# Optimization experiments

Measured on AMD Instinct MI355X. Metric: run time of the kernel, lower is better.

## Reference

```python
import jax, jax.numpy as jnp
import numpy as np

NEG_SLOPE = 0.2

def symlog(v):
    return jnp.sign(v) * jnp.log1p(jnp.abs(v))

def conv1d(v, w, b):
    # v: (N, Cin, L), w: (Cout, Cin, 3), 'same' padding, stride 1
    out = jax.lax.conv_general_dilated(v, w, (1,), 'SAME',
                                       dimension_numbers=('NCH', 'OIH', 'NCH'))
    return out + b[None, :, None]

def glorot(key, shape, fan_in, fan_out):
    s = jnp.sqrt(6.0 / (fan_in + fan_out))
    return jax.random.uniform(key, shape, jnp.float32, -s, s)

def setup_inputs() -> dict:
    N, L, E = 20000, 128, 320000
    IN, H, C, OHC = 512, 8, 32, 8
    key = jax.random.key(0)
    ks = jax.random.split(key, 12)
    x = jax.random.normal(ks[0], (N, IN), jnp.float32)
    onehot = jax.random.uniform(ks[1], (N, L), jnp.float32)
    src = jax.random.randint(ks[2], (E,), 0, N)
    off = jax.random.randint(ks[3], (E,), 1, N)
    dst = (src + off) % N  # guarantees no self loops
    adj = jnp.stack([src, dst], axis=0).astype(jnp.int64)
    lin_w = glorot(ks[4], (IN + OHC, H * C), IN + OHC, H * C)
    att_l = glorot(ks[5], (1, H, C), C, C)
    att_r = glorot(ks[6], (1, H, C), C, C)
    bias = jnp.zeros((H * C,), jnp.float32)
    conv1_w = glorot(ks[7], (8, 1, 3), 3, 24)
    conv1_b = jnp.zeros((8,), jnp.float32)
    conv2_w = glorot(ks[8], (16, 8, 3), 24, 48)
    conv2_b = jnp.zeros((16,), jnp.float32)
    lin2_w = glorot(ks[9], (16, OHC), 16, OHC)
    lin2_b = jnp.zeros((OHC,), jnp.float32)
    return {"x": x, "onehot": onehot, "adj": adj, "n_nodes": N,
            "lin_w": lin_w, "att_l": att_l, "att_r": att_r, "bias": bias,
            "conv1_w": conv1_w, "conv1_b": conv1_b,
            "conv2_w": conv2_w, "conv2_b": conv2_b,
            "lin2_w": lin2_w, "lin2_b": lin2_b}

def reference(x, onehot, adj, n_nodes, lin_w, att_l, att_r, bias,
              conv1_w, conv1_b, conv2_w, conv2_b, lin2_w, lin2_b):
    N = n_nodes
    H, C = att_l.shape[1], att_l.shape[2]
    # one-hot conv pipe: sort -> symlog -> conv-relu x2 -> global avg pool -> linear
    prepared = symlog(jnp.sort(onehot, axis=-1))[:, None, :]  # (N,1,L)
    h = jax.nn.relu(conv1d(prepared, conv1_w, conv1_b))
    h = jax.nn.relu(conv1d(h, conv2_w, conv2_b))
    readout = h.mean(axis=-1) @ lin2_w + lin2_b  # (N, OHC)
    xin = jnp.concatenate([x, readout], axis=-1)
    xh = (xin @ lin_w).reshape(N, H, C)
    al = (xh * att_l).sum(axis=-1)  # (N,H) sending alphas
    ar = (xh * att_r).sum(axis=-1)  # (N,H) receiving alphas
    # add self loops (input adj has none, so remove_self_loops is a no-op)
    loops = jnp.arange(N, dtype=adj.dtype)
    src = jnp.concatenate([adj[0], loops])
    dst = jnp.concatenate([adj[1], loops])
    # GAT-style attention with segment softmax over receiving nodes
    alpha = jax.nn.leaky_relu(al[src] + ar[dst], NEG_SLOPE)  # (Etot,H)
    amax = jax.ops.segment_max(alpha, dst, num_segments=N)
    ex = jnp.exp(alpha - amax[dst])
    denom = jax.ops.segment_sum(ex, dst, num_segments=N)
    alpha = ex / denom[dst]
    # weight + scatter-add aggregate
    wx = xh[src] * alpha[..., None]  # (Etot,H,C)
    new_x = jax.ops.segment_sum(wx, dst, num_segments=N).reshape(N, H * C) + bias
    new_onehot = jax.ops.segment_sum(onehot[src], dst, num_segments=N) + onehot
    return new_x, new_onehot
```

## Files before the change

### kernel.cpp

```cpp
#include <hip/hip_runtime.h>

#define NEG_SLOPE 0.2f

typedef __attribute__((ext_vector_type(4))) float f32x4;
typedef __attribute__((ext_vector_type(2))) float f32x2;
typedef __attribute__((ext_vector_type(8))) short short8;

__device__ __forceinline__ f32x2 mk2(float a, float b) { f32x2 r; r[0] = a; r[1] = b; return r; }

__device__ __forceinline__ f32x2 FMA2(f32x2 a, f32x2 b, f32x2 c) {
#if __has_builtin(__builtin_elementwise_fma)
    return __builtin_elementwise_fma(a, b, c);
#else
    f32x2 r; r[0] = fmaf(a[0], b[0], c[0]); r[1] = fmaf(a[1], b[1], c[1]); return r;
#endif
}

__device__ __forceinline__ ushort f2bf(float f) {
    uint u = __float_as_uint(f);
    u += 0x7FFFu + ((u >> 16) & 1u);
    return (ushort)(u >> 16);
}
__device__ __forceinline__ float bflo(uint u) { return __uint_as_float(u << 16); }
__device__ __forceinline__ float bfhi(uint u) { return __uint_as_float(u & 0xffff0000u); }

__global__ __launch_bounds__(256) void k_conv_wave(
    const float* __restrict__ x, const float* __restrict__ onehot,
    const float* __restrict__ c1w, const float* __restrict__ c1b,
    const float* __restrict__ c2w, const float* __restrict__ c2b,
    const float* __restrict__ l2w, const float* __restrict__ l2b,
    ushort* __restrict__ xpad, uint* __restrict__ ohb, int* __restrict__ cursor, int N) {
    __shared__ ushort Hall[4][1056];

    const int gid = blockIdx.x * 256 + threadIdx.x;
    if (gid < N) cursor[gid] = 0;

    const int wave = threadIdx.x >> 6;
    const int lane = threadIdx.x & 63;
    const int n = blockIdx.x * 4 + wave;
    if (n >= N) return;
    ushort* H = Hall[wave];

    {
        const float* xp = &x[(size_t)n*512 + lane*8];
        float4 lo = *reinterpret_cast<const float4*>(xp);
        float4 hi = *reinterpret_cast<const float4*>(xp + 4);
        uint4 w;
        w.x = (uint)f2bf(lo.x) | ((uint)f2bf(lo.y) << 16);
        w.y = (uint)f2bf(lo.z) | ((uint)f2bf(lo.w) << 16);
        w.z = (uint)f2bf(hi.x) | ((uint)f2bf(hi.y) << 16);
        w.w = (uint)f2bf(hi.z) | ((uint)f2bf(hi.w) << 16);
        *reinterpret_cast<uint4*>(&xpad[(size_t)n*544 + lane*8]) = w;
        if (lane < 3) {
            const uint4 z = make_uint4(0,0,0,0);
            *reinterpret_cast<uint4*>(&xpad[(size_t)n*544 + 520 + lane*8]) = z;
        }
    }

    float2 in2 = *reinterpret_cast<const float2*>(&onehot[(size_t)n * 128 + lane * 2]);
    ohb[(size_t)n*64 + lane] = (uint)f2bf(in2.x) | ((uint)f2bf(in2.y) << 16);
    float v0 = log1pf(in2.x);
    float v1 = log1pf(in2.y);

    #pragma unroll
    for (int k = 2; k <= 128; k <<= 1) {
        const bool asc = ((lane & (k >> 1)) == 0);
        #pragma unroll
        for (int j = k >> 1; j >= 2; j >>= 1) {
            const int m = j >> 1;
            float p0 = __shfl_xor(v0, m, 64);
            float p1 = __shfl_xor(v1, m, 64);
            const bool keepmin = (((lane & m) == 0) == asc);
            v0 = keepmin ? fminf(v0, p0) : fmaxf(v0, p0);
            v1 = keepmin ? fminf(v1, p1) : fmaxf(v1, p1);
        }
        float lo = fminf(v0, v1), hi = fmaxf(v0, v1);
        v0 = asc ? lo : hi;
        v1 = asc ? hi : lo;
    }

    float pm = __shfl_up(v1, 1, 64); if (lane == 0)  pm = 0.f;
    float pp = __shfl_down(v0, 1, 64); if (lane == 63) pp = 0.f;

    float h0[8], h1[8];
    {
        const f32x2 xm = mk2(pm, v0), x0 = mk2(v0, v1), xp2 = mk2(v1, pp);
        #pragma unroll
        for (int c = 0; c < 8; ++c) {
            const float w0 = c1w[c*3+0], w1 = c1w[c*3+1], w2 = c1w[c*3+2], b = c1b[c];
            f32x2 h = FMA2(xm, mk2(w0, w0), FMA2(x0, mk2(w1, w1), FMA2(xp2, mk2(w2, w2), mk2(b, b))));
            h0[c] = fmaxf(h[0], 0.f);
            h1[c] = fmaxf(h[1], 0.f);
        }
    }

    {
        if (lane == 0) {
            const uint4 z = make_uint4(0,0,0,0);
            *reinterpret_cast<uint4*>(&H[0*8])   = z;
            *reinterpret_cast<uint4*>(&H[130*8]) = z;
            *reinterpret_cast<uint4*>(&H[65*8])  = z;
        }
        uint4 w0, w1;
        w0.x = (uint)f2bf(h0[0]) | ((uint)f2bf(h0[1]) << 16);
        w0.y = (uint)f2bf(h0[2]) | ((uint)f2bf(h0[3]) << 16);
        w0.z = (uint)f2bf(h0[4]) | ((uint)f2bf(h0[5]) << 16);
        w0.w = (uint)f2bf(h0[6]) | ((uint)f2bf(h0[7]) << 16);
        w1.x = (uint)f2bf(h1[0]) | ((uint)f2bf(h1[1]) << 16);
        w1.y = (uint)f2bf(h1[2]) | ((uint)f2bf(h1[3]) << 16);
        w1.z = (uint)f2bf(h1[4]) | ((uint)f2bf(h1[5]) << 16);
        w1.w = (uint)f2bf(h1[6]) | ((uint)f2bf(h1[7]) << 16);
        *reinterpret_cast<uint4*>(&H[(66 + lane)*8]) = w0;
        *reinterpret_cast<uint4*>(&H[(lane + 1)*8])  = w1;
    }

    const int co = lane & 15;
    const int g2 = lane >> 4;
    short8 bfrag;
    #pragma unroll
    for (int j = 0; j < 8; ++j) bfrag[j] = 0;
    if (g2 < 3) {
        #pragma unroll
        for (int j = 0; j < 8; ++j) bfrag[j] = (short)f2bf(c2w[(co*8 + j)*3 + g2]);
    }
    const float bias_c = c2b[co];
    const f32x4 zacc = (f32x4)0.f;

    float poolv = 0.f;
    #pragma unroll
    for (int s = 0; s < 8; ++s) {
        const int q = s*16 + co + g2;
        const int slot = (q >> 1) + (q & 1)*66;
        short8 afrag = *reinterpret_cast<const short8*>(&H[slot*8]);
        f32x4 d = __builtin_amdgcn_mfma_f32_16x16x32_bf16(afrag, bfrag, zacc, 0, 0, 0);
        poolv += fmaxf(d[0] + bias_c, 0.f);
        poolv += fmaxf(d[1] + bias_c, 0.f);
        poolv += fmaxf(d[2] + bias_c, 0.f);
        poolv += fmaxf(d[3] + bias_c, 0.f);
    }
    poolv += __shfl_xor(poolv, 16, 64);
    poolv += __shfl_xor(poolv, 32, 64);

    float r = (lane < 8) ? l2b[lane] : 0.f;
    #pragma unroll
    for (int c = 0; c < 16; ++c) {
        float pc = __shfl(poolv, c, 64);
        if (lane < 8) r = fmaf(pc * (1.f/128.f), l2w[c*8 + lane], r);
    }
    if (lane < 8) xpad[(size_t)n*544 + 512 + lane] = f2bf(r);
}

__global__ __launch_bounds__(256) void k_prep(
    const float* __restrict__ lin_w, ushort* __restrict__ Bt,
    const int* __restrict__ dst, int* __restrict__ cursor, int E) {
    const int gid = blockIdx.x * 256 + threadIdx.x;
    if (gid < E) atomicAdd(&cursor[dst[gid]], 1);
    const int col = blockIdx.x;
    if (col < 256) {
        for (int k = threadIdx.x; k < 544; k += 256) {
            float v = (k < 520) ? lin_w[(size_t)k*256 + col] : 0.f;
            Bt[(size_t)col*544 + k] = f2bf(v);
        }
    }
}

__global__ __launch_bounds__(1024) void k_scan(int* __restrict__ deg, int* __restrict__ row_start, int N) {
    __shared__ int wsum[16];
    const int t = threadIdx.x;
    const int w = t >> 6, ln = t & 63;
    const int base = t * 20;
    int v[20];
    int run = 0;
    #pragma unroll
    for (int i = 0; i < 20; ++i) {
        const int idx = base + i;
        int d = 0;
        if (idx < N) { d = deg[idx]; deg[idx] = 0; }
        run += d;
        v[i] = run;
    }
    int s = run;
    #pragma unroll
    for (int d = 1; d < 64; d <<= 1) {
        int u = __shfl_up(s, d, 64);
        if (ln >= d) s += u;
    }
    if (ln == 63) wsum[w] = s;
    __syncthreads();
    if (w == 0) {
        int ws = (ln < 16) ? wsum[ln] : 0;
        int e2 = ws;
        #pragma unroll
        for (int d = 1; d < 16; d <<= 1) {
            int u = __shfl_up(e2, d, 64);
            if (ln >= d) e2 += u;
        }
        if (ln < 16) wsum[ln] = e2 - ws;
    }
    __syncthreads();
    const int off = (s - run) + wsum[w];
    if (t == 0) row_start[0] = 0;
    #pragma unroll
    for (int i = 0; i < 20; ++i) {
        const int idx = base + i;
        if (idx < N) row_start[idx + 1] = off + v[i];
    }
}

__global__ __launch_bounds__(128) void k_gemm_mfma(
    const ushort* __restrict__ xpad, const ushort* __restrict__ Bt,
    const float* __restrict__ att_l, const float* __restrict__ att_r,
    ushort* __restrict__ xhb, float* __restrict__ al, float* __restrict__ ar,
    const int* __restrict__ src, const int* __restrict__ dst,
    const int* __restrict__ row_start, int* __restrict__ cursor, int* __restrict__ csr,
    int N, int E) {
    __shared__ __align__(16) float ep[32*68];

    const int t = threadIdx.x;
    const int wv = t >> 6, lane = t & 63;

    const int nwg = gridDim.x;
    const int q = nwg >> 3, r = nwg & 7;
    const int xcd = blockIdx.x & 7, idx = blockIdx.x >> 3;
    const int logical = (xcd < r ? xcd*(q+1) : r*(q+1) + (xcd-r)*q) + idx;
    const int m0 = (logical >> 2) * 32;
    const int c0 = (logical & 3) * 64;

    const int frow = lane & 15;
    const int fkg  = (lane >> 4) * 8;

    const ushort* ap = &xpad[(size_t)(m0 + wv*16 + frow)*544 + fkg];
    const ushort* bp0 = &Bt[(size_t)(c0 +      frow)*544 + fkg];
    const ushort* bp1 = &Bt[(size_t)(c0 + 16 + frow)*544 + fkg];
    const ushort* bp2 = &Bt[(size_t)(c0 + 32 + frow)*544 + fkg];
    const ushort* bp3 = &Bt[(size_t)(c0 + 48 + frow)*544 + fkg];

    f32x4 acc[4];
    #pragma unroll
    for (int j = 0; j < 4; ++j) acc[j] = (f32x4)0.f;

    short8 afr[2], br0[2], br1[2], br2[2], br3[2];
#define LOADSET(B_, K_)                                                  \
    {                                                                    \
        afr[B_] = *reinterpret_cast<const short8*>(ap  + (K_));          \
        br0[B_] = *reinterpret_cast<const short8*>(bp0 + (K_));          \
        br1[B_] = *reinterpret_cast<const short8*>(bp1 + (K_));          \
        br2[B_] = *reinterpret_cast<const short8*>(bp2 + (K_));          \
        br3[B_] = *reinterpret_cast<const short8*>(bp3 + (K_));          \
    }
    LOADSET(0, 0)
    #pragma unroll
    for (int s = 0; s < 17; ++s) {
        const int b = s & 1;
        if (s + 1 < 17) LOADSET((s + 1) & 1, (s + 1) * 32)
        acc[0] = __builtin_amdgcn_mfma_f32_16x16x32_bf16(afr[b], br0[b], acc[0], 0, 0, 0);
        acc[1] = __builtin_amdgcn_mfma_f32_16x16x32_bf16(afr[b], br1[b], acc[1], 0, 0, 0);
        acc[2] = __builtin_amdgcn_mfma_f32_16x16x32_bf16(afr[b], br2[b], acc[2], 0, 0, 0);
        acc[3] = __builtin_amdgcn_mfma_f32_16x16x32_bf16(afr[b], br3[b], acc[3], 0, 0, 0);
    }
#undef LOADSET

    {
        const int e = blockIdx.x * 128 + t;
        if (e < E) {
            const int d = dst[e];
            const int p = atomicAdd(&cursor[d], 1);
            csr[row_start[d] + p] = src[e];
        }
    }

    {
        const int rb = wv*16 + (lane >> 4)*4;
        const int cb = lane & 15;
        #pragma unroll
        for (int j = 0; j < 4; ++j)
            #pragma unroll
            for (int r2 = 0; r2 < 4; ++r2)
                ep[(rb + r2)*68 + j*16 + cb] = acc[j][r2];
    }
    __syncthreads();
    {
        const int rl = t >> 2;
        const int cq = (t & 3) * 16;
        const int row = m0 + rl;
        if (row < N) {
            const float* s = &ep[rl*68 + cq];
            float vals[16];
            #pragma unroll
            for (int i = 0; i < 16; ++i) vals[i] = s[i];
            uint u[8];
            #pragma unroll
            for (int i = 0; i < 8; ++i)
                u[i] = (uint)f2bf(vals[2*i]) | ((uint)f2bf(vals[2*i+1]) << 16);
            ushort* db = &xhb[(size_t)row*256 + c0 + cq];
            *reinterpret_cast<uint4*>(db)     = make_uint4(u[0], u[1], u[2], u[3]);
            *reinterpret_cast<uint4*>(db + 8) = make_uint4(u[4], u[5], u[6], u[7]);
            float pl = 0.f, pr = 0.f;
            #pragma unroll
            for (int i = 0; i < 16; ++i) {
                pl = fmaf(vals[i], att_l[c0 + cq + i], pl);
                pr = fmaf(vals[i], att_r[c0 + cq + i], pr);
            }
            pl += __shfl_xor(pl, 1, 64);
            pr += __shfl_xor(pr, 1, 64);
            if ((t & 1) == 0) {
                const int head = (c0 >> 5) + ((t & 3) >> 1);
                al[(size_t)row*8 + head] = pl;
                ar[(size_t)row*8 + head] = pr;
            }
        }
    }
}

__global__ __launch_bounds__(256) void k_agg(
    const ushort* __restrict__ xhb,
    const float* __restrict__ al, const float* __restrict__ ar,
    const float* __restrict__ onehot, const uint* __restrict__ ohb,
    const float* __restrict__ bias,
    const int* __restrict__ row_start, const int* __restrict__ csr,
    float* __restrict__ out_x, float* __restrict__ out_oh, int N) {
    const int wave = threadIdx.x >> 6;
    const int lane = threadIdx.x & 63;
    const int n = blockIdx.x * 4 + wave;
    if (n >= N) return;
    const int h = lane >> 3;
    const float ard = ar[(size_t)n*8 + h];

    float a_self = al[(size_t)n*8 + h] + ard;
    a_self = fmaxf(a_self, NEG_SLOPE * a_self);
    float e_self = __expf(a_self);
    uint2 xsb = *reinterpret_cast<const uint2*>(&xhb[(size_t)n*256 + lane*4]);
    float4 acc;
    acc.x = e_self * bflo(xsb.x); acc.y = e_self * bfhi(xsb.x);
    acc.z = e_self * bflo(xsb.y); acc.w = e_self * bfhi(xsb.y);
    float den = e_self;
    float oh0 = 0.f, oh1 = 0.f;

    const int beg = row_start[n], end = row_start[n+1];
    int i = beg;
    for (; i + 3 < end; i += 4) {
        const int s0 = csr[i], s1 = csr[i+1], s2 = csr[i+2], s3 = csr[i+3];
        const float al0 = al[(size_t)s0*8 + h], al1 = al[(size_t)s1*8 + h];
        const float al2 = al[(size_t)s2*8 + h], al3 = al[(size_t)s3*8 + h];
        const uint2 xb0 = *reinterpret_cast<const uint2*>(&xhb[(size_t)s0*256 + lane*4]);
        const uint2 xb1 = *reinterpret_cast<const uint2*>(&xhb[(size_t)s1*256 + lane*4]);
        const uint2 xb2 = *reinterpret_cast<const uint2*>(&xhb[(size_t)s2*256 + lane*4]);
        const uint2 xb3 = *reinterpret_cast<const uint2*>(&xhb[(size_t)s3*256 + lane*4]);
        const uint ob0 = ohb[(size_t)s0*64 + lane];
        const uint ob1 = ohb[(size_t)s1*64 + lane];
        const uint ob2 = ohb[(size_t)s2*64 + lane];
        const uint ob3 = ohb[(size_t)s3*64 + lane];
        float a0 = al0 + ard; a0 = fmaxf(a0, NEG_SLOPE * a0);
        float a1 = al1 + ard; a1 = fmaxf(a1, NEG_SLOPE * a1);
        float a2 = al2 + ard; a2 = fmaxf(a2, NEG_SLOPE * a2);
        float a3 = al3 + ard; a3 = fmaxf(a3, NEG_SLOPE * a3);
        const float e0 = __expf(a0), e1 = __expf(a1), e2 = __expf(a2), e3 = __expf(a3);
        acc.x = fmaf(e0, bflo(xb0.x), fmaf(e1, bflo(xb1.x), fmaf(e2, bflo(xb2.x), fmaf(e3, bflo(xb3.x), acc.x))));
        acc.y = fmaf(e0, bfhi(xb0.x), fmaf(e1, bfhi(xb1.x), fmaf(e2, bfhi(xb2.x), fmaf(e3, bfhi(xb3.x), acc.y))));
        acc.z = fmaf(e0, bflo(xb0.y), fmaf(e1, bflo(xb1.y), fmaf(e2, bflo(xb2.y), fmaf(e3, bflo(xb3.y), acc.z))));
        acc.w = fmaf(e0, bfhi(xb0.y), fmaf(e1, bfhi(xb1.y), fmaf(e2, bfhi(xb2.y), fmaf(e3, bfhi(xb3.y), acc.w))));
        den += (e0 + e1) + (e2 + e3);
        oh0 += (bflo(ob0) + bflo(ob1)) + (bflo(ob2) + bflo(ob3));
        oh1 += (bfhi(ob0) + bfhi(ob1)) + (bfhi(ob2) + bfhi(ob3));
    }
    for (; i < end; ++i) {
        const int s0 = csr[i];
        float a0 = al[(size_t)s0*8 + h] + ard;
        a0 = fmaxf(a0, NEG_SLOPE * a0);
        const float e0 = __expf(a0);
        const uint2 xb0 = *reinterpret_cast<const uint2*>(&xhb[(size_t)s0*256 + lane*4]);
        const uint ob0 = ohb[(size_t)s0*64 + lane];
        acc.x = fmaf(e0, bflo(xb0.x), acc.x);
        acc.y = fmaf(e0, bfhi(xb0.x), acc.y);
        acc.z = fmaf(e0, bflo(xb0.y), acc.z);
        acc.w = fmaf(e0, bfhi(xb0.y), acc.w);
        den += e0;
        oh0 += bflo(ob0);
        oh1 += bfhi(ob0);
    }
    const float inv = 1.f / den;
    const float4 bv = *reinterpret_cast<const float4*>(&bias[lane*4]);
    float4 o;
    o.x = fmaf(acc.x, inv, bv.x);
    o.y = fmaf(acc.y, inv, bv.y);
    o.z = fmaf(acc.z, inv, bv.z);
    o.w = fmaf(acc.w, inv, bv.w);
    *reinterpret_cast<float4*>(&out_x[(size_t)n*256 + lane*4]) = o;
    float2 so = *reinterpret_cast<const float2*>(&onehot[(size_t)n*128 + lane*2]);
    float2 oo;
    oo.x = oh0 + 2.f*so.x;
    oo.y = oh1 + 2.f*so.y;
    *reinterpret_cast<float2*>(&out_oh[(size_t)n*128 + lane*2]) = oo;
}

extern "C" void kernel_launch(void* const* d_in, const int* in_sizes, int n_in,
                              void* d_out, int out_size, void* d_ws, size_t ws_size,
                              hipStream_t stream) {
    const float* x      = (const float*)d_in[0];
    const float* onehot = (const float*)d_in[1];
    const int*   adj    = (const int*)d_in[2];
    const float* lin_w  = (const float*)d_in[4];
    const float* att_l  = (const float*)d_in[5];
    const float* att_r  = (const float*)d_in[6];
    const float* bias   = (const float*)d_in[7];
    const float* c1w    = (const float*)d_in[8];
    const float* c1b    = (const float*)d_in[9];
    const float* c2w    = (const float*)d_in[10];
    const float* c2b    = (const float*)d_in[11];
    const float* l2w    = (const float*)d_in[12];
    const float* l2b    = (const float*)d_in[13];

    const int N = in_sizes[0] / 512;
    const int E = in_sizes[2] / 2;
    const int* src = adj;
    const int* dst = adj + E;

    float* out_x  = (float*)d_out;
    float* out_oh = out_x + (size_t)N * 256;

    ushort* xpad     = (ushort*)d_ws;
    ushort* Bt       = xpad + (size_t)N * 544;
    ushort* xhb      = Bt + (size_t)256 * 544;
    uint*   ohb      = (uint*)(xhb + (size_t)N * 256);
    float*  al       = (float*)(ohb + (size_t)N * 64);
    float*  ar       = al + (size_t)N * 8;
    int*   row_start = (int*)(ar + (size_t)N * 8);
    int*   cursor    = row_start + (N + 1);
    int*   csr       = cursor + N;

    const int EB = (E + 255) / 256;
    const int GB = ((N + 31) / 32) * 4;

    k_conv_wave<<<(N + 3) / 4, 256, 0, stream>>>(x, onehot, c1w, c1b, c2w, c2b, l2w, l2b, xpad, ohb, cursor, N);
    k_prep<<<EB, 256, 0, stream>>>(lin_w, Bt, dst, cursor, E);
    k_scan<<<1, 1024, 0, stream>>>(cursor, row_start, N);
    k_gemm_mfma<<<GB, 128, 0, stream>>>(xpad, Bt, att_l, att_r, xhb, al, ar,
                                        src, dst, row_start, cursor, csr, N, E);
    k_agg<<<(N + 3) / 4, 256, 0, stream>>>(xhb, al, ar, onehot, ohb, bias, row_start, csr, out_x, out_oh, N);
}
```

Measured before the change: 171.7 us.

## Pre-swizzle GEMM operands into MFMA fragment order and double M tile

The conv kernel now writes the bf16 activations directly in a tiled layout matching the MFMA 16x16x32 fragment order, and the weight-prep kernel does the same for the transposed weights. Each lane's fragment load becomes one contiguous 16-byte load. The GEMM tile grows from 32 to 64 rows per block, reusing each B fragment across two A fragments, which halves the grid and doubles the edges each block scatters into the CSR. The cost is a more complex index scheme, padding of N to a multiple of 64, and higher register and LDS use per block.

```diff
diff --git a/kernel.cpp b/kernel.cpp
--- a/kernel.cpp
+++ b/kernel.cpp
@@ -24,12 +24,13 @@
 __device__ __forceinline__ float bflo(uint u) { return __uint_as_float(u << 16); }
 __device__ __forceinline__ float bfhi(uint u) { return __uint_as_float(u & 0xffff0000u); }
 
+
 __global__ __launch_bounds__(256) void k_conv_wave(
     const float* __restrict__ x, const float* __restrict__ onehot,
     const float* __restrict__ c1w, const float* __restrict__ c1b,
     const float* __restrict__ c2w, const float* __restrict__ c2b,
     const float* __restrict__ l2w, const float* __restrict__ l2b,
-    ushort* __restrict__ xpad, uint* __restrict__ ohb, int* __restrict__ cursor, int N) {
+    ushort* __restrict__ xpadA, uint* __restrict__ ohb, int* __restrict__ cursor, int N) {
     __shared__ ushort Hall[4][1056];
 
     const int gid = blockIdx.x * 256 + threadIdx.x;
@@ -40,6 +41,9 @@
     const int n = blockIdx.x * 4 + wave;
     if (n >= N) return;
     ushort* H = Hall[wave];
+
+    const int nt = n >> 6, g16 = (n >> 4) & 3, r16 = n & 15;
+    const size_t qstep = ((size_t)nt*17)*4 + g16;
 
     {
         const float* xp = &x[(size_t)n*512 + lane*8];
@@ -50,11 +54,8 @@
         w.y = (uint)f2bf(lo.z) | ((uint)f2bf(lo.w) << 16);
         w.z = (uint)f2bf(hi.x) | ((uint)f2bf(hi.y) << 16);
         w.w = (uint)f2bf(hi.z) | ((uint)f2bf(hi.w) << 16);
-        *reinterpret_cast<uint4*>(&xpad[(size_t)n*544 + lane*8]) = w;
-        if (lane < 3) {
-            const uint4 z = make_uint4(0,0,0,0);
-            *reinterpret_cast<uint4*>(&xpad[(size_t)n*544 + 520 + lane*8]) = z;
-        }
+        const size_t a = (qstep + (size_t)(lane >> 2)*4)*512 + ((lane & 3)*16 + r16)*8;
+        *reinterpret_cast<uint4*>(&xpadA[a]) = w;
     }
 
     float2 in2 = *reinterpret_cast<const float2*>(&onehot[(size_t)n * 128 + lane * 2]);
@@ -129,8 +130,8 @@
     float poolv = 0.f;
     #pragma unroll
     for (int s = 0; s < 8; ++s) {
-        const int q = s*16 + co + g2;
-        const int slot = (q >> 1) + (q & 1)*66;
+        const int qq = s*16 + co + g2;
+        const int slot = (qq >> 1) + (qq & 1)*66;
         short8 afrag = *reinterpret_cast<const short8*>(&H[slot*8]);
         f32x4 d = __builtin_amdgcn_mfma_f32_16x16x32_bf16(afrag, bfrag, zacc, 0, 0, 0);
         poolv += fmaxf(d[0] + bias_c, 0.f);
@@ -141,25 +142,40 @@
     poolv += __shfl_xor(poolv, 16, 64);
     poolv += __shfl_xor(poolv, 32, 64);
 
-    float r = (lane < 8) ? l2b[lane] : 0.f;
+    float rout = (lane < 8) ? l2b[lane] : 0.f;
     #pragma unroll
     for (int c = 0; c < 16; ++c) {
         float pc = __shfl(poolv, c, 64);
-        if (lane < 8) r = fmaf(pc * (1.f/128.f), l2w[c*8 + lane], r);
-    }
-    if (lane < 8) xpad[(size_t)n*544 + 512 + lane] = f2bf(r);
+        if (lane < 8) rout = fmaf(pc * (1.f/128.f), l2w[c*8 + lane], rout);
+    }
+    {
+        const size_t qb = (qstep + 16u*4u)*512;
+        if (lane < 4) {
+            const int i0 = 2*lane, i1 = 2*lane + 1;
+            float lo = __shfl(rout, i0, 64);
+            float hi = __shfl(rout, i1, 64);
+            uint w = (uint)f2bf(lo) | ((uint)f2bf(hi) << 16);
+            *reinterpret_cast<uint*>(&xpadA[qb + r16*8 + lane*2]) = w;
+        } else if (lane < 7) {
+            const int kc = lane - 3;
+            const uint4 z = make_uint4(0,0,0,0);
+            *reinterpret_cast<uint4*>(&xpadA[qb + (kc*16 + r16)*8]) = z;
+        }
+    }
 }
 
 __global__ __launch_bounds__(256) void k_prep(
-    const float* __restrict__ lin_w, ushort* __restrict__ Bt,
+    const float* __restrict__ lin_w, ushort* __restrict__ BtT,
     const int* __restrict__ dst, int* __restrict__ cursor, int E) {
     const int gid = blockIdx.x * 256 + threadIdx.x;
     if (gid < E) atomicAdd(&cursor[dst[gid]], 1);
     const int col = blockIdx.x;
     if (col < 256) {
+        const int cs = col >> 4, fcol = col & 15;
         for (int k = threadIdx.x; k < 544; k += 256) {
             float v = (k < 520) ? lin_w[(size_t)k*256 + col] : 0.f;
-            Bt[(size_t)col*544 + k] = f2bf(v);
+            const int s = k >> 5, kc = (k >> 3) & 3, j = k & 7;
+            BtT[(size_t)(s*16 + cs)*512 + (kc*16 + fcol)*8 + j] = f2bf(v);
         }
     }
 }
@@ -208,13 +224,13 @@
 }
 
 __global__ __launch_bounds__(128) void k_gemm_mfma(
-    const ushort* __restrict__ xpad, const ushort* __restrict__ Bt,
+    const ushort* __restrict__ xpadA, const ushort* __restrict__ BtT,
     const float* __restrict__ att_l, const float* __restrict__ att_r,
     ushort* __restrict__ xhb, float* __restrict__ al, float* __restrict__ ar,
     const int* __restrict__ src, const int* __restrict__ dst,
     const int* __restrict__ row_start, int* __restrict__ cursor, int* __restrict__ csr,
     int N, int E) {
-    __shared__ __align__(16) float ep[32*68];
+    __shared__ __align__(16) float ep[64*68];
 
     const int t = threadIdx.x;
     const int wv = t >> 6, lane = t & 63;
@@ -223,91 +239,102 @@
     const int q = nwg >> 3, r = nwg & 7;
     const int xcd = blockIdx.x & 7, idx = blockIdx.x >> 3;
     const int logical = (xcd < r ? xcd*(q+1) : r*(q+1) + (xcd-r)*q) + idx;
-    const int m0 = (logical >> 2) * 32;
-    const int c0 = (logical & 3) * 64;
-
-    const int frow = lane & 15;
-    const int fkg  = (lane >> 4) * 8;
-
-    const ushort* ap = &xpad[(size_t)(m0 + wv*16 + frow)*544 + fkg];
-    const ushort* bp0 = &Bt[(size_t)(c0 +      frow)*544 + fkg];
-    const ushort* bp1 = &Bt[(size_t)(c0 + 16 + frow)*544 + fkg];
-    const ushort* bp2 = &Bt[(size_t)(c0 + 32 + frow)*544 + fkg];
-    const ushort* bp3 = &Bt[(size_t)(c0 + 48 + frow)*544 + fkg];
-
-    f32x4 acc[4];
-    #pragma unroll
-    for (int j = 0; j < 4; ++j) acc[j] = (f32x4)0.f;
-
-    short8 afr[2], br0[2], br1[2], br2[2], br3[2];
-#define LOADSET(B_, K_)                                                  \
-    {                                                                    \
-        afr[B_] = *reinterpret_cast<const short8*>(ap  + (K_));          \
-        br0[B_] = *reinterpret_cast<const short8*>(bp0 + (K_));          \
-        br1[B_] = *reinterpret_cast<const short8*>(bp1 + (K_));          \
-        br2[B_] = *reinterpret_cast<const short8*>(bp2 + (K_));          \
-        br3[B_] = *reinterpret_cast<const short8*>(bp3 + (K_));          \
+    const int lt = logical >> 2;
+    const int c0s = (logical & 3) * 4;
+    const int m0 = lt * 64;
+
+    const ushort* A0 = xpadA + ((size_t)(lt*17)*4 + wv*2    )*512 + lane*8;
+    const ushort* A1 = A0 + 512;
+    const ushort* B0 = BtT + (size_t)(c0s + 0)*512 + lane*8;
+    const ushort* B1 = BtT + (size_t)(c0s + 1)*512 + lane*8;
+    const ushort* B2 = BtT + (size_t)(c0s + 2)*512 + lane*8;
+    const ushort* B3 = BtT + (size_t)(c0s + 3)*512 + lane*8;
+
+    f32x4 acc0[4], acc1[4];
+    #pragma unroll
+    for (int j = 0; j < 4; ++j) { acc0[j] = (f32x4)0.f; acc1[j] = (f32x4)0.f; }
+
+    short8 a0[2], a1[2], b0[2], b1[2], b2[2], b3[2];
+#define LOADSET(B_, S_)                                                       \
+    {                                                                         \
+        a0[B_] = *reinterpret_cast<const short8*>(A0 + (size_t)(S_)*2048);    \
+        a1[B_] = *reinterpret_cast<const short8*>(A1 + (size_t)(S_)*2048);    \
+        b0[B_] = *reinterpret_cast<const short8*>(B0 + (size_t)(S_)*8192);    \
+        b1[B_] = *reinterpret_cast<const short8*>(B1 + (size_t)(S_)*8192);    \
+        b2[B_] = *reinterpret_cast<const short8*>(B2 + (size_t)(S_)*8192);    \
+        b3[B_] = *reinterpret_cast<const short8*>(B3 + (size_t)(S_)*8192);    \
     }
     LOADSET(0, 0)
     #pragma unroll
     for (int s = 0; s < 17; ++s) {
         const int b = s & 1;
-        if (s + 1 < 17) LOADSET((s + 1) & 1, (s + 1) * 32)
-        acc[0] = __builtin_amdgcn_mfma_f32_16x16x32_bf16(afr[b], br0[b], acc[0], 0, 0, 0);
-        acc[1] = __builtin_amdgcn_mfma_f32_16x16x32_bf16(afr[b], br1[b], acc[1], 0, 0, 0);
-        acc[2] = __builtin_amdgcn_mfma_f32_16x16x32_bf16(afr[b], br2[b], acc[2], 0, 0, 0);
-        acc[3] = __builtin_amdgcn_mfma_f32_16x16x32_bf16(afr[b], br3[b], acc[3], 0, 0, 0);
+        if (s + 1 < 17) LOADSET((s + 1) & 1, s + 1)
+        acc0[0] = __builtin_amdgcn_mfma_f32_16x16x32_bf16(a0[b], b0[b], acc0[0], 0, 0, 0);
+        acc0[1] = __builtin_amdgcn_mfma_f32_16x16x32_bf16(a0[b], b1[b], acc0[1], 0, 0, 0);
+        acc0[2] = __builtin_amdgcn_mfma_f32_16x16x32_bf16(a0[b], b2[b], acc0[2], 0, 0, 0);
+        acc0[3] = __builtin_amdgcn_mfma_f32_16x16x32_bf16(a0[b], b3[b], acc0[3], 0, 0, 0);
+        acc1[0] = __builtin_amdgcn_mfma_f32_16x16x32_bf16(a1[b], b0[b], acc1[0], 0, 0, 0);
+        acc1[1] = __builtin_amdgcn_mfma_f32_16x16x32_bf16(a1[b], b1[b], acc1[1], 0, 0, 0);
+        acc1[2] = __builtin_amdgcn_mfma_f32_16x16x32_bf16(a1[b], b2[b], acc1[2], 0, 0, 0);
+        acc1[3] = __builtin_amdgcn_mfma_f32_16x16x32_bf16(a1[b], b3[b], acc1[3], 0, 0, 0);
     }
 #undef LOADSET
 
     {
-        const int e = blockIdx.x * 128 + t;
-        if (e < E) {
-            const int d = dst[e];
+        const int e0 = blockIdx.x * 256 + t;
+        if (e0 < E) {
+            const int d = dst[e0];
             const int p = atomicAdd(&cursor[d], 1);
-            csr[row_start[d] + p] = src[e];
-        }
-    }
-
-    {
-        const int rb = wv*16 + (lane >> 4)*4;
+            csr[row_start[d] + p] = src[e0];
+        }
+        const int e1 = e0 + 128;
+        if (e1 < E) {
+            const int d = dst[e1];
+            const int p = atomicAdd(&cursor[d], 1);
+            csr[row_start[d] + p] = src[e1];
+        }
+    }
+
+    {
+        const int rb = wv*32 + ((lane >> 4) * 4);
         const int cb = lane & 15;
         #pragma unroll
         for (int j = 0; j < 4; ++j)
             #pragma unroll
-            for (int r2 = 0; r2 < 4; ++r2)
-                ep[(rb + r2)*68 + j*16 + cb] = acc[j][r2];
+            for (int r2 = 0; r2 < 4; ++r2) {
+                ep[(rb      + r2)*68 + j*16 + cb] = acc0[j][r2];
+                ep[(rb + 16 + r2)*68 + j*16 + cb] = acc1[j][r2];
+            }
     }
     __syncthreads();
     {
-        const int rl = t >> 2;
-        const int cq = (t & 3) * 16;
+        const int rl = t >> 1;
+        const int cq = (t & 1) * 32;
         const int row = m0 + rl;
         if (row < N) {
-            const float* s = &ep[rl*68 + cq];
-            float vals[16];
+            const int c0 = c0s * 16;
+            const float* sp = &ep[rl*68 + cq];
+            float vals[32];
             #pragma unroll
-            for (int i = 0; i < 16; ++i) vals[i] = s[i];
-            uint u[8];
+            for (int i = 0; i < 32; ++i) vals[i] = sp[i];
+            uint u[16];
             #pragma unroll
-            for (int i = 0; i < 8; ++i)
+            for (int i = 0; i < 16; ++i)
                 u[i] = (uint)f2bf(vals[2*i]) | ((uint)f2bf(vals[2*i+1]) << 16);
             ushort* db = &xhb[(size_t)row*256 + c0 + cq];
-            *reinterpret_cast<uint4*>(db)     = make_uint4(u[0], u[1], u[2], u[3]);
-            *reinterpret_cast<uint4*>(db + 8) = make_uint4(u[4], u[5], u[6], u[7]);
+            *reinterpret_cast<uint4*>(db)      = make_uint4(u[0], u[1], u[2], u[3]);
+            *reinterpret_cast<uint4*>(db + 8)  = make_uint4(u[4], u[5], u[6], u[7]);
+            *reinterpret_cast<uint4*>(db + 16) = make_uint4(u[8], u[9], u[10], u[11]);
+            *reinterpret_cast<uint4*>(db + 24) = make_uint4(u[12], u[13], u[14], u[15]);
             float pl = 0.f, pr = 0.f;
             #pragma unroll
-            for (int i = 0; i < 16; ++i) {
+            for (int i = 0; i < 32; ++i) {
                 pl = fmaf(vals[i], att_l[c0 + cq + i], pl);
                 pr = fmaf(vals[i], att_r[c0 + cq + i], pr);
             }
-            pl += __shfl_xor(pl, 1, 64);
-            pr += __shfl_xor(pr, 1, 64);
-            if ((t & 1) == 0) {
-                const int head = (c0 >> 5) + ((t & 3) >> 1);
-                al[(size_t)row*8 + head] = pl;
-                ar[(size_t)row*8 + head] = pr;
-            }
+            const int head = ((c0 + cq) >> 5);
+            al[(size_t)row*8 + head] = pl;
+            ar[(size_t)row*8 + head] = pr;
         }
     }
 }
@@ -418,9 +445,11 @@
     float* out_x  = (float*)d_out;
     float* out_oh = out_x + (size_t)N * 256;
 
-    ushort* xpad     = (ushort*)d_ws;
-    ushort* Bt       = xpad + (size_t)N * 544;
-    ushort* xhb      = Bt + (size_t)256 * 544;
+    const int NT = (N + 63) / 64;
+
+    ushort* xpadA    = (ushort*)d_ws;
+    ushort* BtT      = xpadA + (size_t)NT * 17 * 2048;
+    ushort* xhb      = BtT + (size_t)17 * 8192;
     uint*   ohb      = (uint*)(xhb + (size_t)N * 256);
     float*  al       = (float*)(ohb + (size_t)N * 64);
     float*  ar       = al + (size_t)N * 8;
@@ -429,12 +458,12 @@
     int*   csr       = cursor + N;
 
     const int EB = (E + 255) / 256;
-    const int GB = ((N + 31) / 32) * 4;
-
-    k_conv_wave<<<(N + 3) / 4, 256, 0, stream>>>(x, onehot, c1w, c1b, c2w, c2b, l2w, l2b, xpad, ohb, cursor, N);
-    k_prep<<<EB, 256, 0, stream>>>(lin_w, Bt, dst, cursor, E);
+    const int GB = NT * 4;
+
+    k_conv_wave<<<(N + 3) / 4, 256, 0, stream>>>(x, onehot, c1w, c1b, c2w, c2b, l2w, l2b, xpadA, ohb, cursor, N);
+    k_prep<<<EB, 256, 0, stream>>>(lin_w, BtT, dst, cursor, E);
     k_scan<<<1, 1024, 0, stream>>>(cursor, row_start, N);
-    k_gemm_mfma<<<GB, 128, 0, stream>>>(xpad, Bt, att_l, att_r, xhb, al, ar,
+    k_gemm_mfma<<<GB, 128, 0, stream>>>(xpadA, BtT, att_l, att_r, xhb, al, ar,
                                         src, dst, row_start, cursor, csr, N, E);
     k_agg<<<(N + 3) / 4, 256, 0, stream>>>(xhb, al, ar, onehot, ohb, bias, row_start, csr, out_x, out_oh, N);
 }
```

After: 164.1 us. 1.05x faster.
